# Kernel tuning notes

Measured on AMD Instinct MI355X. Metric: run time of the kernel, lower is better.

Reference implementation:

```python
import jax, jax.numpy as jnp
import numpy as np

HIDDEN = 4096
N_HEADS = 32
N_KV_HEADS = 8
HEAD_DIM = HIDDEN // N_HEADS  # 128
B, S = 2, 4096


def setup_inputs() -> dict:
    key = jax.random.key(0)
    ks = jax.random.split(key, 9)
    sc = 1.0 / np.sqrt(HIDDEN)
    x = jax.random.normal(ks[0], (B, S, HIDDEN), dtype=jnp.float32)
    Wq = jax.random.normal(ks[1], (HIDDEN, HIDDEN), dtype=jnp.float32) * sc
    bq = jax.random.normal(ks[2], (HIDDEN,), dtype=jnp.float32) * 0.01
    Wk = jax.random.normal(ks[3], (N_KV_HEADS * HEAD_DIM, HIDDEN), dtype=jnp.float32) * sc
    bk = jax.random.normal(ks[4], (N_KV_HEADS * HEAD_DIM,), dtype=jnp.float32) * 0.01
    Wv = jax.random.normal(ks[5], (N_KV_HEADS * HEAD_DIM, HIDDEN), dtype=jnp.float32) * sc
    bv = jax.random.normal(ks[6], (N_KV_HEADS * HEAD_DIM,), dtype=jnp.float32) * 0.01
    Wo = jax.random.normal(ks[7], (HIDDEN, HIDDEN), dtype=jnp.float32) * sc
    bo = jax.random.normal(ks[8], (HIDDEN,), dtype=jnp.float32) * 0.01
    return {"x": x, "Wq": Wq, "bq": bq, "Wk": Wk, "bk": bk,
            "Wv": Wv, "bv": bv, "Wo": Wo, "bo": bo}


def reference(x, Wq, bq, Wk, bk, Wv, bv, Wo, bo):
    batch, seq, _ = x.shape
    # Linear projections (torch Linear: x @ W^T + b)
    q = x @ Wq.T + bq                      # [B,S,H*D]
    k = x @ Wk.T + bk                      # [B,S,Hkv*D]
    v = x @ Wv.T + bv
    q = q.reshape(batch, seq, N_HEADS, HEAD_DIM)
    k = k.reshape(batch, seq, N_KV_HEADS, HEAD_DIM)
    v = v.reshape(batch, seq, N_KV_HEADS, HEAD_DIM)
    # GQA handling in source: concatenate [k]*r along head axis (a TILE, not interleave)
    r = N_HEADS // N_KV_HEADS
    k = jnp.tile(k, (1, 1, r, 1))          # [B,S,H,D]
    v = jnp.tile(v, (1, 1, r, 1))
    # Source keeps layout [B,S,H,D]; mx.matmul batches over (B,S), so
    # attention is taken ACROSS THE HEAD AXIS per token (faithful to source).
    scores = jnp.einsum('bshd,bsgd->bshg', q, k) / np.sqrt(HEAD_DIM)  # [B,S,H,H]
    weights = jax.nn.softmax(scores, axis=-1)
    attn = jnp.einsum('bshg,bsgd->bshd', weights, v)  # [B,S,H,D]
    attn = attn.reshape(batch, seq, HIDDEN)
    return attn @ Wo.T + bo
```

## Files before the change

kernel.cpp:

```cpp
#include <hip/hip_runtime.h>
#include <hip/hip_bf16.h>


typedef _Float16 half8 __attribute__((ext_vector_type(8)));
typedef _Float16 half4v __attribute__((ext_vector_type(4)));
typedef float floatx4 __attribute__((ext_vector_type(4)));

#define K_DIM 4096
#define LDAB 8192
#define BM 256
#define BN 256
#define BK 32
#define NSTEP 128

__device__ __forceinline__ void gload16(const void* g, void* l) {
    __builtin_amdgcn_global_load_lds((const __attribute__((address_space(1))) void*)g,
                                     (__attribute__((address_space(3))) void*)l,
                                     16, 0, 0);
}

__global__ __launch_bounds__(256) void split_f32(
    const float* __restrict__ src, _Float16* __restrict__ dst, long long rows) {
    long long n4 = rows * 1024;
    long long stride = (long long)gridDim.x * blockDim.x;
    for (long long i = (long long)blockIdx.x * blockDim.x + threadIdx.x; i < n4; i += stride) {
        float4 v = ((const float4*)src)[i];
        long long r = i >> 10;
        int c = ((int)(i & 1023)) << 2;
        half4v hi, lo;
        hi[0] = (_Float16)v.x; lo[0] = (_Float16)(v.x - (float)hi[0]);
        hi[1] = (_Float16)v.y; lo[1] = (_Float16)(v.y - (float)hi[1]);
        hi[2] = (_Float16)v.z; lo[2] = (_Float16)(v.z - (float)hi[2]);
        hi[3] = (_Float16)v.w; lo[3] = (_Float16)(v.w - (float)hi[3]);
        *(half4v*)&dst[r * LDAB + c] = hi;
        *(half4v*)&dst[r * LDAB + K_DIM + c] = lo;
    }
}

__global__ __launch_bounds__(512, 2) void gemm_split3_8w(
    const _Float16* __restrict__ A, const _Float16* __restrict__ B,
    float* __restrict__ C, const float* __restrict__ bias0,
    const float* __restrict__ bias1, int N) {

    __shared__ __attribute__((aligned(16))) _Float16 lA[2][2][BM * BK];
    __shared__ __attribute__((aligned(16))) _Float16 lB[2][2][BN * BK];

    const int tid = threadIdx.x;
    const int lane = tid & 63;
    const int w = tid >> 6;
    const int wm = w >> 2;
    const int wn = w & 3;

    const int f = blockIdx.x;
    const int nwg = gridDim.x;
    const int lid = (f & 7) * (nwg >> 3) + (f >> 3);
    const long long brow = (long long)(lid & 31) * BM;
    const long long bcol = (long long)(lid >> 5) * BN;

    floatx4 acc[8][4];
#pragma unroll
    for (int m = 0; m < 8; ++m)
#pragma unroll
        for (int n = 0; n < 4; ++n)
            acc[m][n] = (floatx4){0.f, 0.f, 0.f, 0.f};

    const int srow = w * 16 + (lane >> 2);
    const int scol = 8 * ((lane & 3) ^ ((lane >> 3) & 3));
    const _Float16* Asrc = A + (brow + srow) * (long long)LDAB + scol;
    const _Float16* Bsrc = B + (bcol + srow) * (long long)LDAB + scol;

    const int rA = lane & 15;
    const int kcs = 8 * ((lane >> 4) ^ ((lane >> 1) & 3));

    auto stageG1 = [&](int NXT, int ktn) {
        gload16(Asrc + ktn, &lA[NXT][0][w * 512]);
        gload16(Asrc + 128 * (long long)LDAB + ktn, &lA[NXT][0][4096 + w * 512]);
        gload16(Bsrc + ktn, &lB[NXT][0][w * 512]);
        gload16(Bsrc + 128 * (long long)LDAB + ktn, &lB[NXT][0][4096 + w * 512]);
    };
    auto stageG2 = [&](int NXT, int ktn) {
        gload16(Bsrc + K_DIM + ktn, &lB[NXT][1][w * 512]);
        gload16(Bsrc + 128 * (long long)LDAB + K_DIM + ktn, &lB[NXT][1][4096 + w * 512]);
    };
    auto stageG3 = [&](int NXT, int ktn) {
        gload16(Asrc + K_DIM + ktn, &lA[NXT][1][w * 512]);
        gload16(Asrc + 128 * (long long)LDAB + K_DIM + ktn, &lA[NXT][1][4096 + w * 512]);
    };

    stageG1(0, 0);
    stageG2(0, 0);
    stageG3(0, 0);

    auto step = [&](int CUR, int NXT, int ktn) {
        half8 ah[8], bh[4];
        asm volatile("s_waitcnt vmcnt(4)" ::: "memory");
        __builtin_amdgcn_s_barrier();
#pragma unroll
        for (int n = 0; n < 4; ++n)
            bh[n] = *(const half8*)&lB[CUR][0][(wn * 64 + n * 16 + rA) * BK + kcs];
#pragma unroll
        for (int m = 0; m < 8; ++m)
            ah[m] = *(const half8*)&lA[CUR][0][(wm * 128 + m * 16 + rA) * BK + kcs];
        stageG1(NXT, ktn);
        __builtin_amdgcn_s_setprio(1);
#pragma unroll
        for (int m = 0; m < 8; ++m)
#pragma unroll
            for (int n = 0; n < 4; ++n)
                acc[m][n] = __builtin_amdgcn_mfma_f32_16x16x32_f16(
                    ah[m], bh[n], acc[m][n], 0, 0, 0);
        __builtin_amdgcn_s_setprio(0);
        {
            half8 bl[4];
            asm volatile("s_waitcnt vmcnt(6)" ::: "memory");
            __builtin_amdgcn_s_barrier();
#pragma unroll
            for (int n = 0; n < 4; ++n)
                bl[n] = *(const half8*)&lB[CUR][1][(wn * 64 + n * 16 + rA) * BK + kcs];
            stageG2(NXT, ktn);
            __builtin_amdgcn_s_setprio(1);
#pragma unroll
            for (int m = 0; m < 8; ++m)
#pragma unroll
                for (int n = 0; n < 4; ++n)
                    acc[m][n] = __builtin_amdgcn_mfma_f32_16x16x32_f16(
                        ah[m], bl[n], acc[m][n], 0, 0, 0);
            __builtin_amdgcn_s_setprio(0);
        }
        {
            half8 al[8];
            asm volatile("s_waitcnt vmcnt(6)" ::: "memory");
            __builtin_amdgcn_s_barrier();
#pragma unroll
            for (int m = 0; m < 8; ++m)
                al[m] = *(const half8*)&lA[CUR][1][(wm * 128 + m * 16 + rA) * BK + kcs];
            stageG3(NXT, ktn);
            __builtin_amdgcn_s_setprio(1);
#pragma unroll
            for (int m = 0; m < 8; ++m)
#pragma unroll
                for (int n = 0; n < 4; ++n)
                    acc[m][n] = __builtin_amdgcn_mfma_f32_16x16x32_f16(
                        al[m], bh[n], acc[m][n], 0, 0, 0);
            __builtin_amdgcn_s_setprio(0);
        }
    };

    for (int tt = 0; tt < NSTEP; tt += 2) {
        step(0, 1, (tt + 1) * BK);
        step(1, 0, ((tt + 2) & (NSTEP - 1)) * BK);
    }
    asm volatile("s_waitcnt vmcnt(0)" ::: "memory");

    const float* bias = (bias1 != nullptr && bcol >= 1024) ? (bias1 - 1024) : bias0;
    const int crow0 = (lane >> 4) * 4;
    const int ccol = lane & 15;
#pragma unroll
    for (int n = 0; n < 4; ++n) {
        long long col = bcol + wn * 64 + n * 16 + ccol;
        float bv_ = bias[col];
#pragma unroll
        for (int m = 0; m < 8; ++m) {
            long long row = brow + wm * 128 + m * 16 + crow0;
            float* cp = C + row * (long long)N + col;
            __builtin_nontemporal_store(acc[m][n][0] + bv_, cp);
            __builtin_nontemporal_store(acc[m][n][1] + bv_, cp + (long long)N);
            __builtin_nontemporal_store(acc[m][n][2] + bv_, cp + 2LL * N);
            __builtin_nontemporal_store(acc[m][n][3] + bv_, cp + 3LL * N);
        }
    }
}

__global__ __launch_bounds__(256) void attn_token(
    const float* __restrict__ q, const float* __restrict__ kv,
    _Float16* __restrict__ out) {

    const int token = blockIdx.x;
    __shared__ float sQ[32 * 128];
    __shared__ float sK[8 * 128];
    __shared__ float sV[8 * 128];
    __shared__ float sP[32 * 8];

    const int t = threadIdx.x;
    {
        const float4* gq = (const float4*)(q + (long long)token * 4096);
        float4* dq = (float4*)sQ;
        dq[t] = gq[t];
        dq[t + 256] = gq[t + 256];
        dq[t + 512] = gq[t + 512];
        dq[t + 768] = gq[t + 768];
        const float4* gkv = (const float4*)(kv + (long long)token * 2048);
        ((float4*)sK)[t] = gkv[t];
        ((float4*)sV)[t] = gkv[t + 256];
    }
    __syncthreads();

    const int h = t >> 3, j = t & 7;
    const float* qr = sQ + h * 128;
    const float* kr = sK + j * 128;
    float s = 0.f;
#pragma unroll
    for (int i = 0; i < 128; i += 4)
        s += qr[i] * kr[i] + qr[i + 1] * kr[i + 1] +
             qr[i + 2] * kr[i + 2] + qr[i + 3] * kr[i + 3];
    s *= 0.08838834764831845f;

    float mx = s;
    mx = fmaxf(mx, __shfl_xor(mx, 1, 8));
    mx = fmaxf(mx, __shfl_xor(mx, 2, 8));
    mx = fmaxf(mx, __shfl_xor(mx, 4, 8));
    float e = expf(s - mx);
    float sum = e;
    sum += __shfl_xor(sum, 1, 8);
    sum += __shfl_xor(sum, 2, 8);
    sum += __shfl_xor(sum, 4, 8);
    sP[t] = e / sum;
    __syncthreads();

    float p[8];
#pragma unroll
    for (int jj = 0; jj < 8; ++jj) p[jj] = sP[(t >> 3) * 8 + jj];
    const int d0 = (t & 7) * 16;
    const long long obase = (long long)token * LDAB + (t >> 3) * 128;
#pragma unroll
    for (int dd = 0; dd < 16; ++dd) {
        int d = d0 + dd;
        float a = 0.f;
#pragma unroll
        for (int jj = 0; jj < 8; ++jj) a += p[jj] * sV[jj * 128 + d];
        _Float16 hi = (_Float16)a;
        _Float16 lo = (_Float16)(a - (float)hi);
        out[obase + d] = hi;
        out[obase + K_DIM + d] = lo;
    }
}

extern "C" void kernel_launch(void* const* d_in, const int* in_sizes, int n_in,
                              void* d_out, int out_size, void* d_ws, size_t ws_size,
                              hipStream_t stream) {
    const float* x  = (const float*)d_in[0];
    const float* Wq = (const float*)d_in[1];
    const float* bq = (const float*)d_in[2];
    const float* Wk = (const float*)d_in[3];
    const float* bk = (const float*)d_in[4];
    const float* Wv = (const float*)d_in[5];
    const float* bv = (const float*)d_in[6];
    const float* Wo = (const float*)d_in[7];
    const float* bo = (const float*)d_in[8];
    float* out = (float*)d_out;

    char* ws = (char*)d_ws;
    _Float16* A2x  = (_Float16*)(ws + 0);
    _Float16* B2q  = (_Float16*)(ws + 134217728LL);
    _Float16* B2kv = (_Float16*)(ws + 201326592LL);
    _Float16* B2v  = (_Float16*)(ws + 218103808LL);
    _Float16* B2o  = (_Float16*)(ws + 234881024LL);
    float*    qb   = (float*)(ws + 301989888LL);
    float*    kvb  = (float*)(ws + 436207616LL);

    split_f32<<<2048, 256, 0, stream>>>(x,  A2x, 8192);
    split_f32<<<2048, 256, 0, stream>>>(Wq, B2q, 4096);
    split_f32<<<1024, 256, 0, stream>>>(Wk, B2kv, 1024);
    split_f32<<<1024, 256, 0, stream>>>(Wv, B2v, 1024);
    split_f32<<<2048, 256, 0, stream>>>(Wo, B2o, 4096);

    gemm_split3_8w<<<512, 512, 0, stream>>>(A2x, B2q,  qb,  bq, nullptr, 4096);
    gemm_split3_8w<<<256, 512, 0, stream>>>(A2x, B2kv, kvb, bk, bv,      2048);

    attn_token<<<8192, 256, 0, stream>>>(qb, kvb, A2x);

    gemm_split3_8w<<<512, 512, 0, stream>>>(A2x, B2o, out, bo, nullptr, 4096);
}
```

Measured before the change: 2.432 ms.

## Switch GEMM inner loop to 32x32x16 MFMA tiles and merge staging loads

The GEMM microkernel now uses 32x32x16 f16 MFMA instructions on 32x32 accumulator fragments instead of 16x16x32 ones. This cuts the number of LDS fragment reads per MFMA and the instruction count for the same 256x256 block tile. LDS read addressing and the epilogue store mapping are rewritten to match the new fragment layout. The second and third staging loads are merged into one stage with a single barrier, which changes the waitcnt and barrier schedule and risks a different load/compute overlap.

```diff
diff --git a/kernel.cpp b/kernel.cpp
--- a/kernel.cpp
+++ b/kernel.cpp
@@ -4,7 +4,7 @@
 
 typedef _Float16 half8 __attribute__((ext_vector_type(8)));
 typedef _Float16 half4v __attribute__((ext_vector_type(4)));
-typedef float floatx4 __attribute__((ext_vector_type(4)));
+typedef float floatx16 __attribute__((ext_vector_type(16)));
 
 #define K_DIM 4096
 #define LDAB 8192
@@ -57,20 +57,22 @@
     const long long brow = (long long)(lid & 31) * BM;
     const long long bcol = (long long)(lid >> 5) * BN;
 
-    floatx4 acc[8][4];
-#pragma unroll
-    for (int m = 0; m < 8; ++m)
-#pragma unroll
-        for (int n = 0; n < 4; ++n)
-            acc[m][n] = (floatx4){0.f, 0.f, 0.f, 0.f};
+    floatx16 acc[4][2];
+#pragma unroll
+    for (int m = 0; m < 4; ++m)
+#pragma unroll
+        for (int n = 0; n < 2; ++n)
+            acc[m][n] = (floatx16)(0.f);
 
     const int srow = w * 16 + (lane >> 2);
     const int scol = 8 * ((lane & 3) ^ ((lane >> 3) & 3));
     const _Float16* Asrc = A + (brow + srow) * (long long)LDAB + scol;
     const _Float16* Bsrc = B + (bcol + srow) * (long long)LDAB + scol;
 
-    const int rA = lane & 15;
-    const int kcs = 8 * ((lane >> 4) ^ ((lane >> 1) & 3));
+    const int rl = lane & 31;
+    const int rbase8 = ((rl >> 4) * 64 + (rl & 15) * 4) * 8;
+    const int x0 = (((lane >> 5) ^ ((lane >> 1) & 3))) * 8;
+    const int x1 = (((2 + (lane >> 5)) ^ ((lane >> 1) & 3))) * 8;
 
     auto stageG1 = [&](int NXT, int ktn) {
         gload16(Asrc + ktn, &lA[NXT][0][w * 512]);
@@ -78,70 +80,81 @@
         gload16(Bsrc + ktn, &lB[NXT][0][w * 512]);
         gload16(Bsrc + 128 * (long long)LDAB + ktn, &lB[NXT][0][4096 + w * 512]);
     };
-    auto stageG2 = [&](int NXT, int ktn) {
+    auto stageG23 = [&](int NXT, int ktn) {
         gload16(Bsrc + K_DIM + ktn, &lB[NXT][1][w * 512]);
         gload16(Bsrc + 128 * (long long)LDAB + K_DIM + ktn, &lB[NXT][1][4096 + w * 512]);
-    };
-    auto stageG3 = [&](int NXT, int ktn) {
         gload16(Asrc + K_DIM + ktn, &lA[NXT][1][w * 512]);
         gload16(Asrc + 128 * (long long)LDAB + K_DIM + ktn, &lA[NXT][1][4096 + w * 512]);
     };
 
     stageG1(0, 0);
-    stageG2(0, 0);
-    stageG3(0, 0);
+    stageG23(0, 0);
 
     auto step = [&](int CUR, int NXT, int ktn) {
-        half8 ah[8], bh[4];
+        half8 ah[4][2], bh[2][2];
         asm volatile("s_waitcnt vmcnt(4)" ::: "memory");
         __builtin_amdgcn_s_barrier();
 #pragma unroll
-        for (int n = 0; n < 4; ++n)
-            bh[n] = *(const half8*)&lB[CUR][0][(wn * 64 + n * 16 + rA) * BK + kcs];
-#pragma unroll
-        for (int m = 0; m < 8; ++m)
-            ah[m] = *(const half8*)&lA[CUR][0][(wm * 128 + m * 16 + rA) * BK + kcs];
+        for (int nf = 0; nf < 2; ++nf) {
+            bh[nf][0] = *(const half8*)&lB[CUR][0][(wn * 4 + nf * 2) * 512 + rbase8 + x0];
+            bh[nf][1] = *(const half8*)&lB[CUR][0][(wn * 4 + nf * 2) * 512 + rbase8 + x1];
+        }
+#pragma unroll
+        for (int mf = 0; mf < 4; ++mf) {
+            ah[mf][0] = *(const half8*)&lA[CUR][0][(wm * 8 + mf * 2) * 512 + rbase8 + x0];
+            ah[mf][1] = *(const half8*)&lA[CUR][0][(wm * 8 + mf * 2) * 512 + rbase8 + x1];
+        }
         stageG1(NXT, ktn);
         __builtin_amdgcn_s_setprio(1);
 #pragma unroll
-        for (int m = 0; m < 8; ++m)
-#pragma unroll
-            for (int n = 0; n < 4; ++n)
-                acc[m][n] = __builtin_amdgcn_mfma_f32_16x16x32_f16(
-                    ah[m], bh[n], acc[m][n], 0, 0, 0);
+        for (int mf = 0; mf < 4; ++mf)
+#pragma unroll
+            for (int nf = 0; nf < 2; ++nf) {
+                acc[mf][nf] = __builtin_amdgcn_mfma_f32_32x32x16_f16(
+                    ah[mf][0], bh[nf][0], acc[mf][nf], 0, 0, 0);
+                acc[mf][nf] = __builtin_amdgcn_mfma_f32_32x32x16_f16(
+                    ah[mf][1], bh[nf][1], acc[mf][nf], 0, 0, 0);
+            }
         __builtin_amdgcn_s_setprio(0);
+        asm volatile("s_waitcnt vmcnt(4)" ::: "memory");
+        __builtin_amdgcn_s_barrier();
         {
-            half8 bl[4];
-            asm volatile("s_waitcnt vmcnt(6)" ::: "memory");
-            __builtin_amdgcn_s_barrier();
-#pragma unroll
-            for (int n = 0; n < 4; ++n)
-                bl[n] = *(const half8*)&lB[CUR][1][(wn * 64 + n * 16 + rA) * BK + kcs];
-            stageG2(NXT, ktn);
+            half8 bl[2][2];
+#pragma unroll
+            for (int nf = 0; nf < 2; ++nf) {
+                bl[nf][0] = *(const half8*)&lB[CUR][1][(wn * 4 + nf * 2) * 512 + rbase8 + x0];
+                bl[nf][1] = *(const half8*)&lB[CUR][1][(wn * 4 + nf * 2) * 512 + rbase8 + x1];
+            }
+            stageG23(NXT, ktn);
             __builtin_amdgcn_s_setprio(1);
 #pragma unroll
-            for (int m = 0; m < 8; ++m)
-#pragma unroll
-                for (int n = 0; n < 4; ++n)
-                    acc[m][n] = __builtin_amdgcn_mfma_f32_16x16x32_f16(
-                        ah[m], bl[n], acc[m][n], 0, 0, 0);
+            for (int mf = 0; mf < 4; ++mf)
+#pragma unroll
+                for (int nf = 0; nf < 2; ++nf) {
+                    acc[mf][nf] = __builtin_amdgcn_mfma_f32_32x32x16_f16(
+                        ah[mf][0], bl[nf][0], acc[mf][nf], 0, 0, 0);
+                    acc[mf][nf] = __builtin_amdgcn_mfma_f32_32x32x16_f16(
+                        ah[mf][1], bl[nf][1], acc[mf][nf], 0, 0, 0);
+                }
             __builtin_amdgcn_s_setprio(0);
         }
         {
-            half8 al[8];
-            asm volatile("s_waitcnt vmcnt(6)" ::: "memory");
-            __builtin_amdgcn_s_barrier();
-#pragma unroll
-            for (int m = 0; m < 8; ++m)
-                al[m] = *(const half8*)&lA[CUR][1][(wm * 128 + m * 16 + rA) * BK + kcs];
-            stageG3(NXT, ktn);
+            half8 al[4][2];
+#pragma unroll
+            for (int mf = 0; mf < 4; ++mf) {
+                al[mf][0] = *(const half8*)&lA[CUR][1][(wm * 8 + mf * 2) * 512 + rbase8 + x0];
+                al[mf][1] = *(const half8*)&lA[CUR][1][(wm * 8 + mf * 2) * 512 + rbase8 + x1];
+            }
             __builtin_amdgcn_s_setprio(1);
 #pragma unroll
-            for (int m = 0; m < 8; ++m)
-#pragma unroll
-                for (int n = 0; n < 4; ++n)
-                    acc[m][n] = __builtin_amdgcn_mfma_f32_16x16x32_f16(
-                        al[m], bh[n], acc[m][n], 0, 0, 0);
+            for (int mf = 0; mf < 4; ++mf)
+#pragma unroll
+                for (int nf = 0; nf < 2; ++nf) {
+                    acc[mf][nf] = __builtin_amdgcn_mfma_f32_32x32x16_f16(
+                        al[mf][0], bh[nf][0], acc[mf][nf], 0, 0, 0);
+                    acc[mf][nf] = __builtin_amdgcn_mfma_f32_32x32x16_f16(
+                        al[mf][1], bh[nf][1], acc[mf][nf], 0, 0, 0);
+                }
             __builtin_amdgcn_s_setprio(0);
         }
     };
@@ -153,20 +166,22 @@
     asm volatile("s_waitcnt vmcnt(0)" ::: "memory");
 
     const float* bias = (bias1 != nullptr && bcol >= 1024) ? (bias1 - 1024) : bias0;
-    const int crow0 = (lane >> 4) * 4;
-    const int ccol = lane & 15;
-#pragma unroll
-    for (int n = 0; n < 4; ++n) {
-        long long col = bcol + wn * 64 + n * 16 + ccol;
+    const int r0 = 4 * (lane >> 5);
+#pragma unroll
+    for (int nf = 0; nf < 2; ++nf) {
+        long long col = bcol + wn * 64 + nf * 32 + rl;
         float bv_ = bias[col];
 #pragma unroll
-        for (int m = 0; m < 8; ++m) {
-            long long row = brow + wm * 128 + m * 16 + crow0;
-            float* cp = C + row * (long long)N + col;
-            __builtin_nontemporal_store(acc[m][n][0] + bv_, cp);
-            __builtin_nontemporal_store(acc[m][n][1] + bv_, cp + (long long)N);
-            __builtin_nontemporal_store(acc[m][n][2] + bv_, cp + 2LL * N);
-            __builtin_nontemporal_store(acc[m][n][3] + bv_, cp + 3LL * N);
+        for (int mf = 0; mf < 4; ++mf) {
+            long long rowb = brow + wm * 128 + mf * 32 + r0;
+#pragma unroll
+            for (int g = 0; g < 4; ++g)
+#pragma unroll
+                for (int rr = 0; rr < 4; ++rr) {
+                    long long row = rowb + 8 * g + rr;
+                    __builtin_nontemporal_store(acc[mf][nf][g * 4 + rr] + bv_,
+                                                C + row * (long long)N + col);
+                }
         }
     }
 }
```

Result: slower. 2.583 ms (+6.2%).
